# Optimization experiments

Hardware: AMD Instinct MI355X
Metric: run time of the kernel (lower is better)

The kernel has to match this reference:

```python
import jax, jax.numpy as jnp
import numpy as np

B, L, D, H = 2, 2048, 1024, 16
DK = D // H
SCALE = DK ** (-0.25)


def setup_inputs() -> dict:
    key = jax.random.key(0)
    ks = jax.random.split(key, 8)
    return {
        "query": jax.random.normal(ks[0], (B, L, D), jnp.float32),
        "key": jax.random.normal(ks[1], (B, L, D), jnp.float32),
        "value": jax.random.normal(ks[2], (B, L, D), jnp.float32),
        "posbias": jax.random.normal(ks[3], (B, H, L, L), jnp.float32) * 0.1,
        "Wq": jax.random.normal(ks[4], (D, D), jnp.float32) / np.sqrt(D),
        "Wk": jax.random.normal(ks[5], (D, D), jnp.float32) / np.sqrt(D),
        "Wv": jax.random.normal(ks[6], (D, D), jnp.float32) / np.sqrt(D),
        "Wo": jax.random.normal(ks[7], (D, D), jnp.float32) / np.sqrt(D),
    }


def reference(query, key, value, posbias, Wq, Wk, Wv, Wo):
    # nn.Linear(x) = x @ W.T ; weights are [out, in]
    # q: [B, H, L, dk]  k: [B, H, L, dk]  v: [B, H, L, dk]
    q = (query @ Wq.T).reshape(B, L, H, DK).transpose(0, 2, 1, 3) * SCALE
    k = (key @ Wk.T).reshape(B, L, H, DK).transpose(0, 2, 1, 3) * SCALE
    v = (value @ Wv.T).reshape(B, L, H, DK).transpose(0, 2, 1, 3)
    scores = jnp.einsum("bhid,bhjd->bhij", q, k) + posbias  # [B,H,L,L]
    attn = jax.nn.softmax(scores, axis=-1)
    out = jnp.einsum("bhij,bhjd->bhid", attn, v)  # [B,H,L,dk]
    out = out.transpose(0, 2, 1, 3).reshape(B, L, D)
    return out @ Wo.T
```

## Files before the change

kernel.cpp:

```cpp
#include <hip/hip_runtime.h>

#define B_  2
#define L_  2048
#define D_  1024
#define H_  16
#define DK_ 64
#define SCALE_ 0.35355339059327373f

typedef _Float16 f16;
typedef __attribute__((ext_vector_type(8))) _Float16 f16x8;
typedef __attribute__((ext_vector_type(4))) _Float16 f16x4;
typedef __attribute__((ext_vector_type(4))) float    f32x4;

#define AS1C(p) ((const __attribute__((address_space(1))) void*)(p))
#define AS3(p)  ((__attribute__((address_space(3))) void*)(p))

__global__ void cvt_f32_f16(const float* __restrict__ in, f16* __restrict__ out, int n) {
    int i = (blockIdx.x * blockDim.x + threadIdx.x) * 4;
    if (i < n) {
        float4 v = *(const float4*)&in[i];
        f16x4 o;
        o[0] = (f16)v.x; o[1] = (f16)v.y; o[2] = (f16)v.z; o[3] = (f16)v.w;
        *(f16x4*)&out[i] = o;
    }
}

template <typename OutT>
__global__ __launch_bounds__(256) void gemm_bt(
    const f16* __restrict__ A, const f16* __restrict__ Bm, OutT* __restrict__ C,
    int M, int N, int Kd, float alpha)
{
    __shared__ f16 As[128 * 32];
    __shared__ f16 Bs[128 * 32];

    const int tid  = threadIdx.x;
    const int lane = tid & 63;
    const int w    = tid >> 6;
    const int quad = lane >> 4;
    const int l16  = lane & 15;
    const int wm   = w & 1, wn = w >> 1;
    const int m0   = blockIdx.y * 128;
    const int n0   = blockIdx.x * 128;

    f32x4 acc[4][4] = {};

    for (int k0 = 0; k0 < Kd; k0 += 32) {
#pragma unroll
        for (int it = 0; it < 2; ++it) {
            int c    = tid + it * 256;
            int row  = c >> 2;
            int koff = (c & 3) * 8;
            __builtin_amdgcn_global_load_lds(AS1C(&A[(size_t)(m0 + row) * Kd + k0 + koff]),
                                             AS3(&As[c * 8]), 16, 0, 0);
            __builtin_amdgcn_global_load_lds(AS1C(&Bm[(size_t)(n0 + row) * Kd + k0 + koff]),
                                             AS3(&Bs[c * 8]), 16, 0, 0);
        }
        __syncthreads();

        f16x8 af[4], bf[4];
#pragma unroll
        for (int i = 0; i < 4; ++i) {
            af[i] = *(const f16x8*)&As[(wm * 64 + i * 16 + l16) * 32 + quad * 8];
            bf[i] = *(const f16x8*)&Bs[(wn * 64 + i * 16 + l16) * 32 + quad * 8];
        }
#pragma unroll
        for (int i = 0; i < 4; ++i)
#pragma unroll
            for (int j = 0; j < 4; ++j)
                acc[i][j] = __builtin_amdgcn_mfma_f32_16x16x32_f16(af[i], bf[j], acc[i][j], 0, 0, 0);
        __syncthreads();
    }

#pragma unroll
    for (int i = 0; i < 4; ++i)
#pragma unroll
        for (int j = 0; j < 4; ++j)
#pragma unroll
            for (int r = 0; r < 4; ++r) {
                int row = m0 + wm * 64 + i * 16 + quad * 4 + r;
                int col = n0 + wn * 64 + j * 16 + l16;
                C[(size_t)row * N + col] = (OutT)(acc[i][j][r] * alpha);
            }
}

__global__ __launch_bounds__(256) void attn_kernel(
    const f16* __restrict__ Q, const f16* __restrict__ K, const f16* __restrict__ V,
    const float* __restrict__ bias, f16* __restrict__ ctx)
{
    const int qt = blockIdx.x & 31;
    const int h  = (blockIdx.x >> 5) & 15;
    const int b  = blockIdx.x >> 9;
    const int q0 = qt * 64;

    const int tid  = threadIdx.x;
    const int w    = tid >> 6;
    const int lane = tid & 63;
    const int quad = lane >> 4;
    const int l16  = lane & 15;

    __shared__ f16 VT[64][72];
    __shared__ f16 P[4][16][72];

    const size_t bh = (size_t)b * L_ * D_ + (size_t)h * DK_;

    f16x8 qf[2];
    {
        const size_t qrow = (size_t)(q0 + w * 16 + l16);
#pragma unroll
        for (int ks = 0; ks < 2; ++ks)
            qf[ks] = *(const f16x8*)&Q[bh + qrow * D_ + ks * 32 + quad * 8];
    }

    f32x4 oacc[4] = {};
    float m_r[4], l_r[4];
#pragma unroll
    for (int r = 0; r < 4; ++r) { m_r[r] = -1e30f; l_r[r] = 0.f; }

    const float* biasrow = bias + ((size_t)(b * H_ + h) * L_ + q0 + w * 16) * L_;

    for (int j0 = 0; j0 < L_; j0 += 64) {
        {
            int r  = tid >> 2;
            int c0 = (tid & 3) * 16;
            f16x8 v0 = *(const f16x8*)&V[bh + (size_t)(j0 + r) * D_ + c0];
            f16x8 v1 = *(const f16x8*)&V[bh + (size_t)(j0 + r) * D_ + c0 + 8];
#pragma unroll
            for (int i = 0; i < 8; ++i) {
                VT[c0 + i][r]     = v0[i];
                VT[c0 + 8 + i][r] = v1[i];
            }
        }

        f32x4 s[4];
#pragma unroll
        for (int g = 0; g < 4; ++g) {
            const size_t krow = (size_t)(j0 + g * 16 + l16);
            f16x8 kf0 = *(const f16x8*)&K[bh + krow * D_ + quad * 8];
            f16x8 kf1 = *(const f16x8*)&K[bh + krow * D_ + 32 + quad * 8];
            f32x4 a = {};
            a = __builtin_amdgcn_mfma_f32_16x16x32_f16(qf[0], kf0, a, 0, 0, 0);
            a = __builtin_amdgcn_mfma_f32_16x16x32_f16(qf[1], kf1, a, 0, 0, 0);
            s[g] = a;
        }

#pragma unroll
        for (int g = 0; g < 4; ++g)
#pragma unroll
            for (int r = 0; r < 4; ++r)
                s[g][r] += biasrow[(size_t)(quad * 4 + r) * L_ + j0 + g * 16 + l16];

        float alpha[4];
#pragma unroll
        for (int r = 0; r < 4; ++r) {
            float mx = fmaxf(fmaxf(s[0][r], s[1][r]), fmaxf(s[2][r], s[3][r]));
#pragma unroll
            for (int off = 1; off < 16; off <<= 1)
                mx = fmaxf(mx, __shfl_xor(mx, off, 64));
            float mi = fmaxf(m_r[r], mx);
            alpha[r] = __expf(m_r[r] - mi);
            m_r[r]   = mi;
        }
#pragma unroll
        for (int g = 0; g < 4; ++g)
#pragma unroll
            for (int r = 0; r < 4; ++r)
                s[g][r] = __expf(s[g][r] - m_r[r]);
#pragma unroll
        for (int r = 0; r < 4; ++r) {
            float sm = s[0][r] + s[1][r] + s[2][r] + s[3][r];
#pragma unroll
            for (int off = 1; off < 16; off <<= 1)
                sm += __shfl_xor(sm, off, 64);
            l_r[r] = l_r[r] * alpha[r] + sm;
        }
#pragma unroll
        for (int g = 0; g < 4; ++g)
#pragma unroll
            for (int r = 0; r < 4; ++r)
                oacc[g][r] *= alpha[r];

#pragma unroll
        for (int g = 0; g < 4; ++g)
#pragma unroll
            for (int r = 0; r < 4; ++r)
                P[w][quad * 4 + r][g * 16 + l16] = (f16)s[g][r];

        __syncthreads();

#pragma unroll
        for (int ks = 0; ks < 2; ++ks) {
            f16x8 pf = *(const f16x8*)&P[w][l16][ks * 32 + quad * 8];
#pragma unroll
            for (int g = 0; g < 4; ++g) {
                f16x8 vf = *(const f16x8*)&VT[g * 16 + l16][ks * 32 + quad * 8];
                oacc[g] = __builtin_amdgcn_mfma_f32_16x16x32_f16(pf, vf, oacc[g], 0, 0, 0);
            }
        }
        __syncthreads();
    }

#pragma unroll
    for (int g = 0; g < 4; ++g)
#pragma unroll
        for (int r = 0; r < 4; ++r) {
            size_t row = (size_t)(q0 + w * 16 + quad * 4 + r);
            ctx[(size_t)b * L_ * D_ + row * D_ + h * DK_ + g * 16 + l16] =
                (f16)(oacc[g][r] / l_r[r]);
        }
}

extern "C" void kernel_launch(void* const* d_in, const int* in_sizes, int n_in,
                              void* d_out, int out_size, void* d_ws, size_t ws_size,
                              hipStream_t stream)
{
    const float* query = (const float*)d_in[0];
    const float* key   = (const float*)d_in[1];
    const float* value = (const float*)d_in[2];
    const float* pbias = (const float*)d_in[3];
    const float* Wq    = (const float*)d_in[4];
    const float* Wk    = (const float*)d_in[5];
    const float* Wv    = (const float*)d_in[6];
    const float* Wo    = (const float*)d_in[7];
    float* out = (float*)d_out;

    char* ws = (char*)d_ws;
    f16* q16  = (f16*)(ws + 0);
    f16* k16  = (f16*)(ws + 8388608);
    f16* v16  = (f16*)(ws + 16777216);
    f16* wq16 = (f16*)(ws + 25165824);
    f16* wk16 = (f16*)(ws + 27262976);
    f16* wv16 = (f16*)(ws + 29360128);
    f16* wo16 = (f16*)(ws + 31457280);
    f16* Qs   = (f16*)(ws + 33554432);
    f16* Ks   = (f16*)(ws + 41943040);
    f16* Vs   = (f16*)(ws + 50331648);
    f16* ctx  = (f16*)(ws + 58720256);

    const int ML = B_ * L_;
    const int nBig = ML * D_;
    const int nW   = D_ * D_;

    cvt_f32_f16<<<dim3((nBig / 4 + 255) / 256), 256, 0, stream>>>(query, q16, nBig);
    cvt_f32_f16<<<dim3((nBig / 4 + 255) / 256), 256, 0, stream>>>(key,   k16, nBig);
    cvt_f32_f16<<<dim3((nBig / 4 + 255) / 256), 256, 0, stream>>>(value, v16, nBig);
    cvt_f32_f16<<<dim3((nW / 4 + 255) / 256), 256, 0, stream>>>(Wq, wq16, nW);
    cvt_f32_f16<<<dim3((nW / 4 + 255) / 256), 256, 0, stream>>>(Wk, wk16, nW);
    cvt_f32_f16<<<dim3((nW / 4 + 255) / 256), 256, 0, stream>>>(Wv, wv16, nW);
    cvt_f32_f16<<<dim3((nW / 4 + 255) / 256), 256, 0, stream>>>(Wo, wo16, nW);

    dim3 gg(D_ / 128, ML / 128);
    gemm_bt<f16><<<gg, 256, 0, stream>>>(q16, wq16, Qs, ML, D_, D_, SCALE_);
    gemm_bt<f16><<<gg, 256, 0, stream>>>(k16, wk16, Ks, ML, D_, D_, SCALE_);
    gemm_bt<f16><<<gg, 256, 0, stream>>>(v16, wv16, Vs, ML, D_, D_, 1.0f);

    attn_kernel<<<dim3(B_ * H_ * (L_ / 64)), 256, 0, stream>>>(Qs, Ks, Vs, pbias, ctx);

    gemm_bt<float><<<gg, 256, 0, stream>>>(ctx, wo16, out, ML, D_, D_, 1.0f);
}
```

Baseline: 953.3 us.

## Batch conversions and projections, double-buffer GEMM, prefetch V and raise MFMA priority

The seven f32-to-f16 conversion launches are merged into two launches indexed by blockIdx.z, and the three QKV projection GEMMs are merged into one grid-z launch. The GEMM now double-buffers its LDS tiles so the next K-tile's global-to-LDS load overlaps the current tile's MFMAs. The attention kernel issues the V global loads early and writes the transposed tile to LDS only after the softmax, hiding load latency. s_setprio hints are wrapped around the MFMA sections. The changes cut launch overhead and latency stalls at the cost of more LDS and register use.

```diff
diff --git a/kernel.cpp b/kernel.cpp
--- a/kernel.cpp
+++ b/kernel.cpp
@@ -15,7 +15,12 @@
 #define AS1C(p) ((const __attribute__((address_space(1))) void*)(p))
 #define AS3(p)  ((__attribute__((address_space(3))) void*)(p))
 
-__global__ void cvt_f32_f16(const float* __restrict__ in, f16* __restrict__ out, int n) {
+struct CvtArgs { const float* in[4]; f16* out[4]; };
+
+__global__ void cvt_f32_f16(CvtArgs a, int n) {
+    const int z = blockIdx.z;
+    const float* __restrict__ in = a.in[z];
+    f16* __restrict__ out = a.out[z];
     int i = (blockIdx.x * blockDim.x + threadIdx.x) * 4;
     if (i < n) {
         float4 v = *(const float4*)&in[i];
@@ -26,12 +31,12 @@
 }
 
 template <typename OutT>
-__global__ __launch_bounds__(256) void gemm_bt(
+__device__ __forceinline__ void gemm_bt_body(
     const f16* __restrict__ A, const f16* __restrict__ Bm, OutT* __restrict__ C,
     int M, int N, int Kd, float alpha)
 {
-    __shared__ f16 As[128 * 32];
-    __shared__ f16 Bs[128 * 32];
+    __shared__ f16 As[2][128 * 32];
+    __shared__ f16 Bs[2][128 * 32];
 
     const int tid  = threadIdx.x;
     const int lane = tid & 63;
@@ -43,32 +48,45 @@
     const int n0   = blockIdx.x * 128;
 
     f32x4 acc[4][4] = {};
-
-    for (int k0 = 0; k0 < Kd; k0 += 32) {
+    const int nt = Kd >> 5;
+
+    auto stage = [&](int t, int buf) {
+        const int k0 = t * 32;
 #pragma unroll
         for (int it = 0; it < 2; ++it) {
-            int c    = tid + it * 256;
-            int row  = c >> 2;
-            int koff = (c & 3) * 8;
+            int cc   = tid + it * 256;
+            int row  = cc >> 2;
+            int koff = (cc & 3) * 8;
             __builtin_amdgcn_global_load_lds(AS1C(&A[(size_t)(m0 + row) * Kd + k0 + koff]),
-                                             AS3(&As[c * 8]), 16, 0, 0);
+                                             AS3(&As[buf][cc * 8]), 16, 0, 0);
             __builtin_amdgcn_global_load_lds(AS1C(&Bm[(size_t)(n0 + row) * Kd + k0 + koff]),
-                                             AS3(&Bs[c * 8]), 16, 0, 0);
-        }
-        __syncthreads();
+                                             AS3(&Bs[buf][cc * 8]), 16, 0, 0);
+        }
+    };
+
+    stage(0, 0);
+    __syncthreads();
+    int cur = 0;
+
+    for (int t = 0; t < nt; ++t) {
+        if (t + 1 < nt) stage(t + 1, cur ^ 1);
 
         f16x8 af[4], bf[4];
 #pragma unroll
         for (int i = 0; i < 4; ++i) {
-            af[i] = *(const f16x8*)&As[(wm * 64 + i * 16 + l16) * 32 + quad * 8];
-            bf[i] = *(const f16x8*)&Bs[(wn * 64 + i * 16 + l16) * 32 + quad * 8];
-        }
+            af[i] = *(const f16x8*)&As[cur][(wm * 64 + i * 16 + l16) * 32 + quad * 8];
+            bf[i] = *(const f16x8*)&Bs[cur][(wn * 64 + i * 16 + l16) * 32 + quad * 8];
+        }
+        __builtin_amdgcn_s_setprio(1);
 #pragma unroll
         for (int i = 0; i < 4; ++i)
 #pragma unroll
             for (int j = 0; j < 4; ++j)
                 acc[i][j] = __builtin_amdgcn_mfma_f32_16x16x32_f16(af[i], bf[j], acc[i][j], 0, 0, 0);
+        __builtin_amdgcn_s_setprio(0);
+
         __syncthreads();
+        cur ^= 1;
     }
 
 #pragma unroll
@@ -81,6 +99,24 @@
                 int col = n0 + wn * 64 + j * 16 + l16;
                 C[(size_t)row * N + col] = (OutT)(acc[i][j][r] * alpha);
             }
+}
+
+struct ProjArgs {
+    const f16* A[3];
+    const f16* Bm[3];
+    f16*       C[3];
+    float      alpha[3];
+};
+
+__global__ __launch_bounds__(256) void gemm_proj3(ProjArgs p, int M, int N, int Kd) {
+    const int z = blockIdx.z;
+    gemm_bt_body<f16>(p.A[z], p.Bm[z], p.C[z], M, N, Kd, p.alpha[z]);
+}
+
+__global__ __launch_bounds__(256) void gemm_out(
+    const f16* __restrict__ A, const f16* __restrict__ Bm, float* __restrict__ C,
+    int M, int N, int Kd, float alpha) {
+    gemm_bt_body<float>(A, Bm, C, M, N, Kd, alpha);
 }
 
 __global__ __launch_bounds__(256) void attn_kernel(
@@ -119,19 +155,13 @@
     const float* biasrow = bias + ((size_t)(b * H_ + h) * L_ + q0 + w * 16) * L_;
 
     for (int j0 = 0; j0 < L_; j0 += 64) {
-        {
-            int r  = tid >> 2;
-            int c0 = (tid & 3) * 16;
-            f16x8 v0 = *(const f16x8*)&V[bh + (size_t)(j0 + r) * D_ + c0];
-            f16x8 v1 = *(const f16x8*)&V[bh + (size_t)(j0 + r) * D_ + c0 + 8];
-#pragma unroll
-            for (int i = 0; i < 8; ++i) {
-                VT[c0 + i][r]     = v0[i];
-                VT[c0 + 8 + i][r] = v1[i];
-            }
-        }
+        const int vr  = tid >> 2;
+        const int vc0 = (tid & 3) * 16;
+        f16x8 v0 = *(const f16x8*)&V[bh + (size_t)(j0 + vr) * D_ + vc0];
+        f16x8 v1 = *(const f16x8*)&V[bh + (size_t)(j0 + vr) * D_ + vc0 + 8];
 
         f32x4 s[4];
+        __builtin_amdgcn_s_setprio(1);
 #pragma unroll
         for (int g = 0; g < 4; ++g) {
             const size_t krow = (size_t)(j0 + g * 16 + l16);
@@ -142,6 +172,7 @@
             a = __builtin_amdgcn_mfma_f32_16x16x32_f16(qf[1], kf1, a, 0, 0, 0);
             s[g] = a;
         }
+        __builtin_amdgcn_s_setprio(0);
 
 #pragma unroll
         for (int g = 0; g < 4; ++g)
@@ -185,8 +216,15 @@
             for (int r = 0; r < 4; ++r)
                 P[w][quad * 4 + r][g * 16 + l16] = (f16)s[g][r];
 
+#pragma unroll
+        for (int i = 0; i < 8; ++i) {
+            VT[vc0 + i][vr]     = v0[i];
+            VT[vc0 + 8 + i][vr] = v1[i];
+        }
+
         __syncthreads();
 
+        __builtin_amdgcn_s_setprio(1);
 #pragma unroll
         for (int ks = 0; ks < 2; ++ks) {
             f16x8 pf = *(const f16x8*)&P[w][l16][ks * 32 + quad * 8];
@@ -196,6 +234,7 @@
                 oacc[g] = __builtin_amdgcn_mfma_f32_16x16x32_f16(pf, vf, oacc[g], 0, 0, 0);
             }
         }
+        __builtin_amdgcn_s_setprio(0);
         __syncthreads();
     }
 
@@ -240,20 +279,29 @@
     const int nBig = ML * D_;
     const int nW   = D_ * D_;
 
-    cvt_f32_f16<<<dim3((nBig / 4 + 255) / 256), 256, 0, stream>>>(query, q16, nBig);
-    cvt_f32_f16<<<dim3((nBig / 4 + 255) / 256), 256, 0, stream>>>(key,   k16, nBig);
-    cvt_f32_f16<<<dim3((nBig / 4 + 255) / 256), 256, 0, stream>>>(value, v16, nBig);
-    cvt_f32_f16<<<dim3((nW / 4 + 255) / 256), 256, 0, stream>>>(Wq, wq16, nW);
-    cvt_f32_f16<<<dim3((nW / 4 + 255) / 256), 256, 0, stream>>>(Wk, wk16, nW);
-    cvt_f32_f16<<<dim3((nW / 4 + 255) / 256), 256, 0, stream>>>(Wv, wv16, nW);
-    cvt_f32_f16<<<dim3((nW / 4 + 255) / 256), 256, 0, stream>>>(Wo, wo16, nW);
-
-    dim3 gg(D_ / 128, ML / 128);
-    gemm_bt<f16><<<gg, 256, 0, stream>>>(q16, wq16, Qs, ML, D_, D_, SCALE_);
-    gemm_bt<f16><<<gg, 256, 0, stream>>>(k16, wk16, Ks, ML, D_, D_, SCALE_);
-    gemm_bt<f16><<<gg, 256, 0, stream>>>(v16, wv16, Vs, ML, D_, D_, 1.0f);
+    {
+        CvtArgs a{};
+        a.in[0] = query; a.in[1] = key; a.in[2] = value;
+        a.out[0] = q16;  a.out[1] = k16; a.out[2] = v16;
+        cvt_f32_f16<<<dim3((nBig / 4 + 255) / 256, 1, 3), 256, 0, stream>>>(a, nBig);
+    }
+    {
+        CvtArgs a{};
+        a.in[0] = Wq;   a.in[1] = Wk;   a.in[2] = Wv;   a.in[3] = Wo;
+        a.out[0] = wq16; a.out[1] = wk16; a.out[2] = wv16; a.out[3] = wo16;
+        cvt_f32_f16<<<dim3((nW / 4 + 255) / 256, 1, 4), 256, 0, stream>>>(a, nW);
+    }
+
+    {
+        ProjArgs p{};
+        p.A[0] = q16;  p.A[1] = k16;  p.A[2] = v16;
+        p.Bm[0] = wq16; p.Bm[1] = wk16; p.Bm[2] = wv16;
+        p.C[0] = Qs;   p.C[1] = Ks;   p.C[2] = Vs;
+        p.alpha[0] = SCALE_; p.alpha[1] = SCALE_; p.alpha[2] = 1.0f;
+        gemm_proj3<<<dim3(D_ / 128, ML / 128, 3), 256, 0, stream>>>(p, ML, D_, D_);
+    }
 
     attn_kernel<<<dim3(B_ * H_ * (L_ / 64)), 256, 0, stream>>>(Qs, Ks, Vs, pbias, ctx);
 
-    gemm_bt<float><<<gg, 256, 0, stream>>>(ctx, wo16, out, ML, D_, D_, 1.0f);
-}
+    gemm_out<<<dim3(D_ / 128, ML / 128), 256, 0, stream>>>(ctx, wo16, out, ML, D_, D_, 1.0f);
+}
```

After: 893.5 us. -6.3%, faster.
